# Performance work log

Measured on AMD Instinct MI355X. Metric: run time of the kernel, lower is better.

Reference implementation:

```python
import jax, jax.numpy as jnp
import numpy as np

INPUT_DIM, HIDDEN, LATENT = 17, 512, 256
B, T = 4096, 512


def setup_inputs() -> dict:
    key = jax.random.key(0)
    ks = jax.random.split(key, 16)
    s = 0.02
    inp = {
        "x": jax.random.normal(ks[0], (B, T, INPUT_DIM), dtype=jnp.float32),
        "h0": jnp.zeros((B, HIDDEN), dtype=jnp.float32),
        # encoder: Linear(17->256), ReLU, Linear(256->256), ReLU
        "enc_w1": jax.random.normal(ks[1], (LATENT, INPUT_DIM)) * s,
        "enc_b1": jnp.zeros((LATENT,), jnp.float32),
        "enc_w2": jax.random.normal(ks[2], (LATENT, LATENT)) * s,
        "enc_b2": jnp.zeros((LATENT,), jnp.float32),
        # GRUCell(latent+1 -> hidden): gates ordered [r, z, n] as in torch
        "w_ih": jax.random.normal(ks[3], (3 * HIDDEN, LATENT + 1)) * s,
        "w_hh": jax.random.normal(ks[4], (3 * HIDDEN, HIDDEN)) * s,
        "b_ih": jnp.zeros((3 * HIDDEN,), jnp.float32),
        "b_hh": jnp.zeros((3 * HIDDEN,), jnp.float32),
        "q_w": jax.random.normal(ks[5], (4, HIDDEN)) * s,
        "q_b": jnp.zeros((4,), jnp.float32),
        "v_w": jax.random.normal(ks[6], (3, HIDDEN)) * s,
        "v_b": jnp.zeros((3,), jnp.float32),
        "c_w": jax.random.normal(ks[7], (3, HIDDEN)) * s,
        "c_b": jnp.zeros((3,), jnp.float32),
    }
    return inp


def _quat_to_rotmat(q):
    # q: [B, 4] = [w, x, y, z] -> R: [B, 3, 3]
    w, x, y, z = q[:, 0], q[:, 1], q[:, 2], q[:, 3]
    xx, yy, zz = x * x, y * y, z * z
    xy, xz, yz = x * y, x * z, y * z
    wx, wy, wz = w * x, w * y, w * z
    r0 = jnp.stack([1 - 2 * (yy + zz), 2 * (xy - wz), 2 * (xz + wy)], axis=-1)
    r1 = jnp.stack([2 * (xy + wz), 1 - 2 * (xx + zz), 2 * (yz - wx)], axis=-1)
    r2 = jnp.stack([2 * (xz - wy), 2 * (yz + wx), 1 - 2 * (xx + yy)], axis=-1)
    return jnp.stack([r0, r1, r2], axis=1)


def _gru_cell(xin, h, w_ih, w_hh, b_ih, b_hh):
    gi = xin @ w_ih.T + b_ih  # [B, 3H]
    gh = h @ w_hh.T + b_hh
    i_r, i_z, i_n = jnp.split(gi, 3, axis=-1)
    h_r, h_z, h_n = jnp.split(gh, 3, axis=-1)
    r = jax.nn.sigmoid(i_r + h_r)
    z = jax.nn.sigmoid(i_z + h_z)
    n = jnp.tanh(i_n + r * h_n)
    return (1.0 - z) * n + z * h


def _forward(x, h0, enc_w1, enc_b1, enc_w2, enc_b2, w_ih, w_hh, b_ih, b_hh,
             q_w, q_b, v_w, v_b, c_w, c_b):
    xt = jnp.swapaxes(x, 0, 1)  # [T, B, 17]

    def step(carry, x_t):
        h, dp = carry
        dt = x_t[:, -1:]                      # [B, 1]
        acc = x_t[:, 0:3]                     # [B, 3]
        z1 = jax.nn.relu(x_t @ enc_w1.T + enc_b1)
        lat = jax.nn.relu(z1 @ enc_w2.T + enc_b2)
        gin = jnp.concatenate([lat, dt], axis=-1)
        h = _gru_cell(gin, h, w_ih, w_hh, b_ih, b_hh)
        q_raw = h @ q_w.T + q_b
        # F.normalize(p=2, eps=1e-12)
        q = q_raw / jnp.maximum(jnp.linalg.norm(q_raw, axis=-1, keepdims=True), 1e-12)
        v_world = h @ v_w.T + v_b
        R = _quat_to_rotmat(q)
        acc_world = jnp.einsum('bij,bj->bi', R, acc)
        dp_baseline = v_world * dt + 0.5 * acc_world * dt * dt
        eps = h @ c_w.T + c_b
        dp = dp + dp_baseline + eps
        return (h, dp), None

    total_dp0 = jnp.zeros((x.shape[0], 3), dtype=x.dtype)
    (h_f, total_dp), _ = jax.lax.scan(step, (h0, total_dp0), xt)
    return total_dp


def reference(x, h0, enc_w1, enc_b1, enc_w2, enc_b2, w_ih, w_hh, b_ih, b_hh,
              q_w, q_b, v_w, v_b, c_w, c_b):
    return _forward(x, h0, enc_w1, enc_b1, enc_w2, enc_b2, w_ih, w_hh, b_ih,
                    b_hh, q_w, q_b, v_w, v_b, c_w, c_b)
```

## Files before the change

kernel.cpp:

```cpp
#include <hip/hip_runtime.h>
#include <math.h>

#define T_STEPS 512
#define IN_DIM  17
#define HID     512
#define LAT     256
#define BT      16
#define NTH     512
#define CHUNK   4

typedef __attribute__((ext_vector_type(8))) _Float16 half8;
typedef __attribute__((ext_vector_type(4))) float    f32x4;

#define OFF_HB0   0
#define OFF_HB1   4194304
#define OFF_LAT   8388608
#define OFF_WG    16777216
#define OFF_W2P   19136512
#define OFF_W1P   19267584
#define OFF_HEADP 19283968
#define OFF_W256  19300352
#define OFF_BCOMB 19306496
#define OFF_BHN   19312640
#define OFF_DT    19314688
#define OFF_CTR   19380224

static __device__ inline unsigned short f2h(float f) {
    union { _Float16 h; unsigned short u; } cv;
    cv.h = (_Float16)f;
    return cv.u;
}

__global__ void pack_kernel(const float* __restrict__ enc_w1,
                            const float* __restrict__ enc_w2,
                            const float* __restrict__ w_ih,
                            const float* __restrict__ w_hh,
                            const float* __restrict__ b_ih,
                            const float* __restrict__ b_hh,
                            const float* __restrict__ q_w,
                            const float* __restrict__ v_w,
                            const float* __restrict__ c_w,
                            const float* __restrict__ h0,
                            unsigned char* __restrict__ ws) {
    unsigned short* wgP   = (unsigned short*)(ws + OFF_WG);
    unsigned short* w2P   = (unsigned short*)(ws + OFF_W2P);
    unsigned short* w1P   = (unsigned short*)(ws + OFF_W1P);
    unsigned short* headP = (unsigned short*)(ws + OFF_HEADP);
    unsigned short* hb0   = (unsigned short*)(ws + OFF_HB0);
    float* w256  = (float*)(ws + OFF_W256);
    float* bcomb = (float*)(ws + OFF_BCOMB);
    float* bhn   = (float*)(ws + OFF_BHN);
    unsigned int* ctr = (unsigned int*)(ws + OFF_CTR);

    const int tid = blockIdx.x * blockDim.x + threadIdx.x;
    const int stride = gridDim.x * blockDim.x;

    for (int idx = tid; idx < 32 * 24 * 3 * 64 * 8; idx += stride) {
        int j = idx & 7, l = (idx >> 3) & 63;
        int r = idx >> 9;
        int g = r % 3; r /= 3;
        int kt = r % 24; int s = r / 24;
        int row = g * 512 + s * 16 + (l & 15);
        int kk  = ((l >> 4) & 3) * 8 + j;
        float v;
        if (kt < 8) v = w_ih[(size_t)row * 257 + (kt * 32 + kk)];
        else        v = w_hh[(size_t)row * 512 + ((kt - 8) * 32 + kk)];
        wgP[idx] = f2h(v);
    }
    for (int idx = tid; idx < 16 * 8 * 64 * 8; idx += stride) {
        int j = idx & 7, l = (idx >> 3) & 63, kt = (idx >> 9) & 7, nt = idx >> 12;
        int n = nt * 16 + (l & 15);
        int k = kt * 32 + ((l >> 4) & 3) * 8 + j;
        w2P[idx] = f2h(enc_w2[(size_t)n * 256 + k]);
    }
    for (int idx = tid; idx < 16 * 64 * 8; idx += stride) {
        int j = idx & 7, l = (idx >> 3) & 63, nt = idx >> 9;
        int n = nt * 16 + (l & 15);
        int k = ((l >> 4) & 3) * 8 + j;
        w1P[idx] = (k < IN_DIM) ? f2h(enc_w1[(size_t)n * IN_DIM + k]) : (unsigned short)0;
    }
    for (int idx = tid; idx < 16 * 64 * 8; idx += stride) {
        int j = idx & 7, l = (idx >> 3) & 63, kt = idx >> 9;
        int d = l & 15;
        int k = kt * 32 + ((l >> 4) & 3) * 8 + j;
        float v = 0.f;
        if (d < 4)       v = q_w[(size_t)d * HID + k];
        else if (d < 7)  v = v_w[(size_t)(d - 4) * HID + k];
        else if (d < 10) v = c_w[(size_t)(d - 7) * HID + k];
        headP[idx] = f2h(v);
    }
    for (int idx = tid; idx < 1536; idx += stride) {
        w256[idx]  = w_ih[(size_t)idx * 257 + 256];
        bcomb[idx] = (idx < 1024) ? (b_ih[idx] + b_hh[idx]) : b_ih[idx];
    }
    for (int idx = tid; idx < 512; idx += stride) bhn[idx] = b_hh[1024 + idx];
    for (int idx = tid; idx < 4096 * 512; idx += stride) {
        int c  = idx & 15;
        int r  = (idx >> 4) & 511;
        int sg = idx >> 13;
        int gg = sg >> 5, ss = sg & 31;
        hb0[idx] = f2h(h0[((size_t)(gg * 512 + r)) * 512 + ss * 16 + c]);
    }
    for (int idx = tid; idx < 5128; idx += stride) ctr[idx] = 0;
}

#define MFMA16(a, b, c) __builtin_amdgcn_mfma_f32_16x16x32_f16((a), (b), (c), 0, 0, 0)

static __device__ inline void bar_arrive(unsigned int* slot) {
    __syncthreads();
    if (threadIdx.x == 0)
        __hip_atomic_fetch_add(slot, 1u, __ATOMIC_RELAXED, __HIP_MEMORY_SCOPE_AGENT);
}
static __device__ inline void bar_wait(unsigned int* slot) {
    if (threadIdx.x == 0) {
        unsigned int spins = 0;
        while (__hip_atomic_load(slot, __ATOMIC_RELAXED, __HIP_MEMORY_SCOPE_AGENT) < 32u) {
            __builtin_amdgcn_s_sleep(2);
            if (++spins > 100000000u) break;
        }
    }
    __syncthreads();
    asm volatile("buffer_inv sc0" ::: "memory");
}
static __device__ inline void xcd_barrier(unsigned int* slot) {
    bar_arrive(slot);
    bar_wait(slot);
}

__global__ __launch_bounds__(NTH, 2)
void imu_coop_kernel(const float* __restrict__ x,
                     const float* __restrict__ h0,
                     const float* __restrict__ enc_b1,
                     const float* __restrict__ enc_b2,
                     const float* __restrict__ q_b,
                     const float* __restrict__ v_b,
                     const float* __restrict__ c_b,
                     unsigned char* __restrict__ ws,
                     float* __restrict__ out)
{
    __shared__ __align__(16) unsigned short wgL[24 * 3 * 64 * 8];
    __shared__ __align__(16) unsigned short headL[16 * 64 * 8];
    __shared__ __align__(16) unsigned short xbf64[64][32];
    __shared__ __align__(16) unsigned short z1bf64[64][264];
    __shared__ __align__(16) float          sdotP[8][16][17];
    __shared__ float eb1L[256], eb2L[256];
    __shared__ float dtL[512][4];
    __shared__ float xownL[2][4][16][4];
    __shared__ int   s_slS;

    unsigned short* hb[2] = { (unsigned short*)(ws + OFF_HB0),
                              (unsigned short*)(ws + OFF_HB1) };
    unsigned short*       latbuf = (unsigned short*)(ws + OFF_LAT);
    const unsigned short* wgP    = (const unsigned short*)(ws + OFF_WG);
    const unsigned short* w2P    = (const unsigned short*)(ws + OFF_W2P);
    const unsigned short* w1P    = (const unsigned short*)(ws + OFF_W1P);
    const unsigned short* headP  = (const unsigned short*)(ws + OFF_HEADP);
    const float* w256g = (const float*)(ws + OFF_W256);
    const float* bcmg  = (const float*)(ws + OFF_BCOMB);
    const float* bhng  = (const float*)(ws + OFF_BHN);
    float* dtbuf = (float*)(ws + OFF_DT);

    const int t    = threadIdx.x;
    const int w    = t >> 6;
    const int l    = t & 63;
    const int l15  = l & 15;
    const int lq   = (l >> 4) & 3;
    const int lqh  = lq >> 1;
    const int c8   = (lq & 1) * 8;

    unsigned int xcc;
    asm volatile("s_getreg_b32 %0, hwreg(HW_REG_XCC_ID)" : "=s"(xcc));
    const int g = (int)(xcc & 7u);
    if (t == 0) {
        unsigned int* tk = (unsigned int*)(ws + OFF_CTR) + 5120 + g;
        s_slS = (int)(__hip_atomic_fetch_add(tk, 1u, __ATOMIC_RELAXED,
                                             __HIP_MEMORY_SCOPE_AGENT) & 31u);
    }
    __syncthreads();
    const int s_sl = s_slS;
    const int eb0  = g * 512 + s_sl * 16;

    unsigned int* stepctr  = (unsigned int*)(ws + OFF_CTR) + (size_t)g * 512;
    unsigned int* chunkctr = (unsigned int*)(ws + OFF_CTR + 16384) + (size_t)g * 128;

    const f32x4 fz = {0.f, 0.f, 0.f, 0.f};

    {
        const uint4* src = (const uint4*)(wgP + (size_t)s_sl * (24 * 3 * 64 * 8));
        uint4* dst = (uint4*)wgL;
        for (int i = t; i < 24 * 3 * 64; i += NTH) dst[i] = src[i];
    }
    {
        const uint4* src = (const uint4*)headP;
        uint4* dst = (uint4*)headL;
        for (int i = t; i < 16 * 64; i += NTH) dst[i] = src[i];
    }
    for (int idx = t; idx < 256; idx += NTH) { eb1L[idx] = enc_b1[idx]; eb2L[idx] = enc_b2[idx]; }
    for (int idx = t; idx < 64 * 32; idx += NTH) xbf64[idx >> 5][idx & 31] = 0;

    const float qb0 = q_b[0], qb1 = q_b[1], qb2 = q_b[2], qb3 = q_b[3];
    const float vb0 = v_b[0], vb1 = v_b[1], vb2 = v_b[2];
    const float cb0 = c_b[0], cb1 = c_b[1], cb2 = c_b[2];

    const int jd = s_sl * 16 + l15;
    const float bR  = bcmg[jd],        bZ  = bcmg[512 + jd];
    const float bIN = bcmg[1024 + jd], bHN = bhng[jd];
    const float wr2 = w256g[jd], wz2 = w256g[512 + jd], wn2 = w256g[1024 + jd];

    float ho[4][4];
    #pragma unroll
    for (int mt = 0; mt < 4; ++mt)
        #pragma unroll
        for (int i = 0; i < 4; ++i)
            ho[mt][i] = h0[(size_t)(g * 512 + w * 64 + mt * 16 + lq * 4 + i) * HID + jd];

    float dp0 = 0.f, dp1 = 0.f, dp2 = 0.f;
    __syncthreads();

    const size_t r0 = (size_t)(g * 512 + w * 64) + l15;

#define LDA_L(dst, ktv)                                                         \
            { _Pragma("unroll")                                                 \
              for (int mt = 0; mt < 4; ++mt)                                    \
                  dst[mt] = *(const half8*)(latp + (size_t)mt * (16 * 4 * 256) + (ktv) * 32); }
#define LDA_H(dst, ktv)                                                         \
            { _Pragma("unroll")                                                 \
              for (int mt = 0; mt < 4; ++mt)                                    \
                  dst[mt] = *(const half8*)(hA + (size_t)((ktv) - 8) * 16384 + mt * 256); }
#define LDB(dst, ktv)                                                           \
            { _Pragma("unroll")                                                 \
              for (int gg = 0; gg < 3; ++gg)                                    \
                  dst[gg] = *(const half8*)&wgL[(((ktv) * 3 + gg) * 64 + l) * 8]; }
#define DOMF_L(A, B)                                                            \
            { _Pragma("unroll")                                                 \
              for (int mt = 0; mt < 4; ++mt) {                                  \
                  aR[mt]  = MFMA16(A[mt], B[0], aR[mt]);                        \
                  aZ[mt]  = MFMA16(A[mt], B[1], aZ[mt]);                        \
                  aNi[mt] = MFMA16(A[mt], B[2], aNi[mt]); } }
#define DOMF_H(A, B)                                                            \
            { _Pragma("unroll")                                                 \
              for (int mt = 0; mt < 4; ++mt) {                                  \
                  aR[mt]  = MFMA16(A[mt], B[0], aR[mt]);                        \
                  aZ[mt]  = MFMA16(A[mt], B[1], aZ[mt]);                        \
                  aNh[mt] = MFMA16(A[mt], B[2], aNh[mt]); } }

    for (int s = 0; s < T_STEPS; ++s) {
        const int cs = s & 3;
        const int rp = s & 1, wp = rp ^ 1;
        const unsigned short* hgx = hb[rp] + (size_t)g * 262144;
        unsigned short*       hwx = hb[wp] + (size_t)g * 262144 + (size_t)s_sl * 8192;

        if (cs == 0) {
            if (s > 0) bar_wait(&stepctr[s - 1]);
            const int c = s >> 2;
            for (int idx = t; idx < 17 * 16 * CHUNK; idx += NTH) {
                int k = idx % 17, rem = idx / 17;
                int b = rem & 15, cc = rem >> 4;
                float v = x[((size_t)(eb0 + b) * T_STEPS + (c * 4 + cc)) * IN_DIM + k];
                xbf64[cc * 16 + b][k] = f2h(v);
                if (k < 3) xownL[c & 1][cc][b][k] = v;
                if (k == 16) {
                    dtbuf[(size_t)(eb0 + b) * 4 + cc] = v;
                    xownL[c & 1][cc][b][3] = v;
                }
            }
            __syncthreads();
            {
                const int nt0 = 2 * w, nt1 = 2 * w + 1;
                half8 bv0 = *(const half8*)(w1P + ((size_t)nt0 * 64 + l) * 8);
                half8 bv1 = *(const half8*)(w1P + ((size_t)nt1 * 64 + l) * 8);
                f32x4 e[4][2];
                #pragma unroll
                for (int mt = 0; mt < 4; ++mt) {
                    half8 av = *(const half8*)&xbf64[mt * 16 + l15][lq * 8];
                    e[mt][0] = MFMA16(av, bv0, fz);
                    e[mt][1] = MFMA16(av, bv1, fz);
                }
                __syncthreads();
                #pragma unroll
                for (int mt = 0; mt < 4; ++mt)
                    #pragma unroll
                    for (int i = 0; i < 4; ++i) {
                        int m64 = mt * 16 + lq * 4 + i;
                        int n0 = nt0 * 16 + l15, n1 = nt1 * 16 + l15;
                        z1bf64[m64][n0] = f2h(fmaxf(e[mt][0][i] + eb1L[n0], 0.f));
                        z1bf64[m64][n1] = f2h(fmaxf(e[mt][1][i] + eb1L[n1], 0.f));
                    }
            }
            __syncthreads();
            {
                const int nt0 = 2 * w, nt1 = 2 * w + 1;
                f32x4 e[4][2];
                #pragma unroll
                for (int mt = 0; mt < 4; ++mt) { e[mt][0] = fz; e[mt][1] = fz; }
                #pragma unroll
                for (int kt = 0; kt < 8; ++kt) {
                    half8 bv0 = *(const half8*)(w2P + ((size_t)(nt0 * 8 + kt) * 64 + l) * 8);
                    half8 bv1 = *(const half8*)(w2P + ((size_t)(nt1 * 8 + kt) * 64 + l) * 8);
                    #pragma unroll
                    for (int mt = 0; mt < 4; ++mt) {
                        half8 av = *(const half8*)&z1bf64[mt * 16 + l15][kt * 32 + lq * 8];
                        e[mt][0] = MFMA16(av, bv0, e[mt][0]);
                        e[mt][1] = MFMA16(av, bv1, e[mt][1]);
                    }
                }
                #pragma unroll
                for (int mt = 0; mt < 4; ++mt)
                    #pragma unroll
                    for (int i = 0; i < 4; ++i) {
                        int b = lq * 4 + i;
                        int n0 = nt0 * 16 + l15, n1 = nt1 * 16 + l15;
                        size_t rb = ((size_t)(eb0 + b) * 4 + mt) * 256;
                        latbuf[rb + n0] = f2h(fmaxf(e[mt][0][i] + eb2L[n0], 0.f));
                        latbuf[rb + n1] = f2h(fmaxf(e[mt][1][i] + eb2L[n1], 0.f));
                    }
            }
            xcd_barrier(&chunkctr[c]);
            {
                const float* srcdt = dtbuf + (size_t)g * 2048;
                float* dstdt = &dtL[0][0];
                for (int idx = t; idx < 2048; idx += NTH) dstdt[idx] = srcdt[idx];
            }
            __syncthreads();
        }

        f32x4 aR[4], aZ[4], aNi[4], aNh[4];
        #pragma unroll
        for (int mt = 0; mt < 4; ++mt) { aR[mt] = fz; aZ[mt] = fz; aNi[mt] = fz; aNh[mt] = fz; }

        {
            const unsigned short* latp = latbuf + (r0 * 4 + cs) * 256 + lq * 8;
            half8 aF[3][4], bF[2][3];
            LDA_L(aF[0], 0); LDA_L(aF[1], 1); LDA_L(aF[2], 2);
            LDB(bF[0], 0); LDB(bF[1], 1);
            #pragma unroll
            for (int kt = 0; kt < 8; ++kt) {
                DOMF_L(aF[kt % 3], bF[kt & 1]);
                if (kt < 5) LDA_L(aF[kt % 3], kt + 3);
                if (kt < 6) LDB(bF[kt & 1], kt + 2);
            }
        }

        if (cs != 0 && s > 0) bar_wait(&stepctr[s - 1]);

        const unsigned short* hA = hgx + (size_t)lqh * 8192
                                       + (size_t)(w * 64 + l15) * 16 + c8;
        half8 aF[3][4], bF[2][3];
        LDA_H(aF[0], 8); LDA_H(aF[1], 9); LDA_H(aF[2], 10);
        LDB(bF[0], 8); LDB(bF[1], 9);

        if (s > 0) {
            f32x4 hc = fz;
            const int ka = 2 * w, kb = 2 * w + 1;
            const unsigned short* hH = hgx + (size_t)(s_sl * 16 + l15) * 16 + c8;
            half8 a0 = *(const half8*)(hH + (size_t)(2 * ka + lqh) * 8192);
            half8 b0 = *(const half8*)(headL + ((size_t)ka * 64 + l) * 8);
            half8 a1 = *(const half8*)(hH + (size_t)(2 * kb + lqh) * 8192);
            half8 b1 = *(const half8*)(headL + ((size_t)kb * 64 + l) * 8);
            hc = MFMA16(a0, b0, hc);
            hc = MFMA16(a1, b1, hc);
            #pragma unroll
            for (int i = 0; i < 4; ++i) sdotP[w][lq * 4 + i][l15] = hc[i];
            __syncthreads();
            if (t < BT) {
                const int b = t;
                float sd[10];
                #pragma unroll
                for (int d = 0; d < 10; ++d) {
                    float acc = 0.f;
                    #pragma unroll
                    for (int w8 = 0; w8 < 8; ++w8) acc += sdotP[w8][b][d];
                    sd[d] = acc;
                }
                const int ps = s - 1, pcc = ps & 3, ppar = (ps >> 2) & 1;
                float ax = xownL[ppar][pcc][b][0], ay = xownL[ppar][pcc][b][1];
                float az = xownL[ppar][pcc][b][2], dtv = xownL[ppar][pcc][b][3];
                float q0 = sd[0] + qb0, q1 = sd[1] + qb1;
                float q2 = sd[2] + qb2, q3 = sd[3] + qb3;
                float nrm = fmaxf(sqrtf(q0*q0 + q1*q1 + q2*q2 + q3*q3), 1e-12f);
                float qw = q0/nrm, qx = q1/nrm, qy = q2/nrm, qz = q3/nrm;
                float vx = sd[4] + vb0, vy = sd[5] + vb1, vz = sd[6] + vb2;
                float ex = sd[7] + cb0, ey = sd[8] + cb1, ez = sd[9] + cb2;
                float xx = qx*qx, yy = qy*qy, zz = qz*qz;
                float xy = qx*qy, xz = qx*qz, yz = qy*qz;
                float wxq = qw*qx, wyq = qw*qy, wzq = qw*qz;
                float aw0 = (1.f - 2.f*(yy+zz))*ax + 2.f*(xy-wzq)*ay + 2.f*(xz+wyq)*az;
                float aw1 = 2.f*(xy+wzq)*ax + (1.f - 2.f*(xx+zz))*ay + 2.f*(yz-wxq)*az;
                float aw2 = 2.f*(xz-wyq)*ax + 2.f*(yz+wxq)*ay + (1.f - 2.f*(xx+yy))*az;
                float hdt2 = 0.5f * dtv * dtv;
                dp0 += vx*dtv + aw0*hdt2 + ex;
                dp1 += vy*dtv + aw1*hdt2 + ey;
                dp2 += vz*dtv + aw2*hdt2 + ez;
            }
        }

        #pragma unroll
        for (int k2 = 0; k2 < 16; ++k2) {
            DOMF_H(aF[k2 % 3], bF[k2 & 1]);
            if (k2 < 13) LDA_H(aF[k2 % 3], k2 + 11);
            if (k2 < 14) LDB(bF[k2 & 1], k2 + 10);
        }

        #pragma unroll
        for (int mt = 0; mt < 4; ++mt) {
            #pragma unroll
            for (int i = 0; i < 4; ++i) {
                const int rl = w * 64 + mt * 16 + lq * 4 + i;
                float dtv = dtL[rl][cs];
                float gr = aR[mt][i]  + bR  + dtv * wr2;
                float gz = aZ[mt][i]  + bZ  + dtv * wz2;
                float gi = aNi[mt][i] + bIN + dtv * wn2;
                float gh = aNh[mt][i] + bHN;
                float r  = 1.f / (1.f + __expf(-gr));
                float zg = 1.f / (1.f + __expf(-gz));
                float narg = gi + r * gh;
                float n  = 1.f - 2.f / (__expf(2.f * narg) + 1.f);
                float hn = (1.f - zg) * n + zg * ho[mt][i];
                ho[mt][i] = hn;
                hwx[rl * 16 + l15] = f2h(hn);
            }
        }
        bar_arrive(&stepctr[s]);
    }
#undef LDA_L
#undef LDA_H
#undef LDB
#undef DOMF_L
#undef DOMF_H

    bar_wait(&stepctr[T_STEPS - 1]);
    {
        const unsigned short* hgx = hb[T_STEPS & 1] + (size_t)g * 262144;
        f32x4 hc = fz;
        const int ka = 2 * w, kb = 2 * w + 1;
        const unsigned short* hH = hgx + (size_t)(s_sl * 16 + l15) * 16 + c8;
        half8 a0 = *(const half8*)(hH + (size_t)(2 * ka + lqh) * 8192);
        half8 b0 = *(const half8*)(headL + ((size_t)ka * 64 + l) * 8);
        half8 a1 = *(const half8*)(hH + (size_t)(2 * kb + lqh) * 8192);
        half8 b1 = *(const half8*)(headL + ((size_t)kb * 64 + l) * 8);
        hc = MFMA16(a0, b0, hc);
        hc = MFMA16(a1, b1, hc);
        #pragma unroll
        for (int i = 0; i < 4; ++i) sdotP[w][lq * 4 + i][l15] = hc[i];
    }
    __syncthreads();
    if (t < BT) {
        const int b = t;
        float sd[10];
        #pragma unroll
        for (int d = 0; d < 10; ++d) {
            float acc = 0.f;
            #pragma unroll
            for (int w8 = 0; w8 < 8; ++w8) acc += sdotP[w8][b][d];
            sd[d] = acc;
        }
        const int pcc = (T_STEPS - 1) & 3, ppar = ((T_STEPS - 1) >> 2) & 1;
        float ax = xownL[ppar][pcc][b][0], ay = xownL[ppar][pcc][b][1];
        float az = xownL[ppar][pcc][b][2], dtv = xownL[ppar][pcc][b][3];
        float q0 = sd[0] + qb0, q1 = sd[1] + qb1;
        float q2 = sd[2] + qb2, q3 = sd[3] + qb3;
        float nrm = fmaxf(sqrtf(q0*q0 + q1*q1 + q2*q2 + q3*q3), 1e-12f);
        float qw = q0/nrm, qx = q1/nrm, qy = q2/nrm, qz = q3/nrm;
        float vx = sd[4] + vb0, vy = sd[5] + vb1, vz = sd[6] + vb2;
        float ex = sd[7] + cb0, ey = sd[8] + cb1, ez = sd[9] + cb2;
        float xx = qx*qx, yy = qy*qy, zz = qz*qz;
        float xy = qx*qy, xz = qx*qz, yz = qy*qz;
        float wxq = qw*qx, wyq = qw*qy, wzq = qw*qz;
        float aw0 = (1.f - 2.f*(yy+zz))*ax + 2.f*(xy-wzq)*ay + 2.f*(xz+wyq)*az;
        float aw1 = 2.f*(xy+wzq)*ax + (1.f - 2.f*(xx+zz))*ay + 2.f*(yz-wxq)*az;
        float aw2 = 2.f*(xz-wyq)*ax + 2.f*(yz+wxq)*ay + (1.f - 2.f*(xx+yy))*az;
        float hdt2 = 0.5f * dtv * dtv;
        dp0 += vx*dtv + aw0*hdt2 + ex;
        dp1 += vy*dtv + aw1*hdt2 + ey;
        dp2 += vz*dtv + aw2*hdt2 + ez;
        out[(size_t)(eb0 + b) * 3 + 0] = dp0;
        out[(size_t)(eb0 + b) * 3 + 1] = dp1;
        out[(size_t)(eb0 + b) * 3 + 2] = dp2;
    }
}

extern "C" void kernel_launch(void* const* d_in, const int* in_sizes, int n_in,
                              void* d_out, int out_size, void* d_ws, size_t ws_size,
                              hipStream_t stream) {
    const float* x      = (const float*)d_in[0];
    const float* h0     = (const float*)d_in[1];
    const float* enc_w1 = (const float*)d_in[2];
    const float* enc_b1 = (const float*)d_in[3];
    const float* enc_w2 = (const float*)d_in[4];
    const float* enc_b2 = (const float*)d_in[5];
    const float* w_ih   = (const float*)d_in[6];
    const float* w_hh   = (const float*)d_in[7];
    const float* b_ih   = (const float*)d_in[8];
    const float* b_hh   = (const float*)d_in[9];
    const float* q_w    = (const float*)d_in[10];
    const float* q_b    = (const float*)d_in[11];
    const float* v_w    = (const float*)d_in[12];
    const float* v_b    = (const float*)d_in[13];
    const float* c_w    = (const float*)d_in[14];
    const float* c_b    = (const float*)d_in[15];
    unsigned char* ws = (unsigned char*)d_ws;
    float* out = (float*)d_out;

    hipLaunchKernelGGL(pack_kernel, dim3(2048), dim3(256), 0, stream,
                       enc_w1, enc_w2, w_ih, w_hh, b_ih, b_hh, q_w, v_w, c_w, h0, ws);

    void* args[] = { (void*)&x, (void*)&h0, (void*)&enc_b1, (void*)&enc_b2,
                     (void*)&q_b, (void*)&v_b, (void*)&c_b, (void*)&ws, (void*)&out };
    (void)hipLaunchCooperativeKernel((void*)imu_coop_kernel, dim3(256), dim3(NTH),
                                     args, 0, stream);
}
```

Measured before the change: 12.14 ms.

## Replace counter barriers with per-block tag slots and prefetch encoder chunk

Swaps the atomic-increment step and chunk counters for per-block monotonic tag slots, which 32 lanes poll in parallel, so each barrier costs one plain store instead of a contended atomic add. The encoder MLP for the next chunk now runs right after a step's arrive, overlapping the wait on other blocks, and its results sit in registers until the next chunk's latent write. It also spreads the 10-way head reduction across 160 threads and deepens the h-load prefetch ring from 3 to 4. The cost is more register pressure from the held encoder accumulators and the larger prefetch ring, plus subtle ordering risk around the latent buffer and dt staging.

```diff
diff --git a/kernel.cpp b/kernel.cpp
--- a/kernel.cpp
+++ b/kernel.cpp
@@ -101,30 +101,27 @@
         int gg = sg >> 5, ss = sg & 31;
         hb0[idx] = f2h(h0[((size_t)(gg * 512 + r)) * 512 + ss * 16 + c]);
     }
-    for (int idx = tid; idx < 5128; idx += stride) ctr[idx] = 0;
+    for (int idx = tid; idx < 4096; idx += stride) ctr[idx] = 0;
 }
 
 #define MFMA16(a, b, c) __builtin_amdgcn_mfma_f32_16x16x32_f16((a), (b), (c), 0, 0, 0)
 
-static __device__ inline void bar_arrive(unsigned int* slot) {
+static __device__ inline void tag_arrive(unsigned int* slot, int ss, unsigned int tag) {
     __syncthreads();
     if (threadIdx.x == 0)
-        __hip_atomic_fetch_add(slot, 1u, __ATOMIC_RELAXED, __HIP_MEMORY_SCOPE_AGENT);
+        __hip_atomic_store(slot + ss, tag, __ATOMIC_RELAXED, __HIP_MEMORY_SCOPE_AGENT);
 }
-static __device__ inline void bar_wait(unsigned int* slot) {
-    if (threadIdx.x == 0) {
+static __device__ inline void tag_wait(unsigned int* slot, unsigned int tag) {
+    if (threadIdx.x < 32) {
+        const int lane = (int)threadIdx.x;
         unsigned int spins = 0;
-        while (__hip_atomic_load(slot, __ATOMIC_RELAXED, __HIP_MEMORY_SCOPE_AGENT) < 32u) {
-            __builtin_amdgcn_s_sleep(2);
-            if (++spins > 100000000u) break;
+        while (__hip_atomic_load(slot + lane, __ATOMIC_RELAXED, __HIP_MEMORY_SCOPE_AGENT) < tag) {
+            __builtin_amdgcn_s_sleep(1);
+            if (++spins > 50000000u) break;
         }
     }
     __syncthreads();
     asm volatile("buffer_inv sc0" ::: "memory");
-}
-static __device__ inline void xcd_barrier(unsigned int* slot) {
-    bar_arrive(slot);
-    bar_wait(slot);
 }
 
 __global__ __launch_bounds__(NTH, 2)
@@ -146,6 +143,7 @@
     __shared__ float eb1L[256], eb2L[256];
     __shared__ float dtL[512][4];
     __shared__ float xownL[2][4][16][4];
+    __shared__ float sdS[16][10];
     __shared__ int   s_slS;
 
     unsigned short* hb[2] = { (unsigned short*)(ws + OFF_HB0),
@@ -172,7 +170,7 @@
     asm volatile("s_getreg_b32 %0, hwreg(HW_REG_XCC_ID)" : "=s"(xcc));
     const int g = (int)(xcc & 7u);
     if (t == 0) {
-        unsigned int* tk = (unsigned int*)(ws + OFF_CTR) + 5120 + g;
+        unsigned int* tk = (unsigned int*)(ws + OFF_CTR) + 2048 + g;
         s_slS = (int)(__hip_atomic_fetch_add(tk, 1u, __ATOMIC_RELAXED,
                                              __HIP_MEMORY_SCOPE_AGENT) & 31u);
     }
@@ -180,8 +178,8 @@
     const int s_sl = s_slS;
     const int eb0  = g * 512 + s_sl * 16;
 
-    unsigned int* stepctr  = (unsigned int*)(ws + OFF_CTR) + (size_t)g * 512;
-    unsigned int* chunkctr = (unsigned int*)(ws + OFF_CTR + 16384) + (size_t)g * 128;
+    unsigned int* stepslot  = (unsigned int*)(ws + OFF_CTR) + (size_t)g * 32;
+    unsigned int* chunkslot = (unsigned int*)(ws + OFF_CTR + 4096) + (size_t)g * 32;
 
     const f32x4 fz = {0.f, 0.f, 0.f, 0.f};
 
@@ -215,9 +213,76 @@
             ho[mt][i] = h0[(size_t)(g * 512 + w * 64 + mt * 16 + lq * 4 + i) * HID + jd];
 
     float dp0 = 0.f, dp1 = 0.f, dp2 = 0.f;
+    f32x4 eReg[4][2];
     __syncthreads();
 
     const size_t r0 = (size_t)(g * 512 + w * 64) + l15;
+
+#define STAGE_CHUNK(cchunk)                                                          \
+  { const int c_ = (cchunk);                                                         \
+    for (int idx = t; idx < 17 * 16 * CHUNK; idx += NTH) {                           \
+        int k = idx % 17, rem = idx / 17;                                            \
+        int b = rem & 15, cc = rem >> 4;                                             \
+        float v = x[((size_t)(eb0 + b) * T_STEPS + (c_ * 4 + cc)) * IN_DIM + k];     \
+        xbf64[cc * 16 + b][k] = f2h(v);                                              \
+        if (k < 3) xownL[c_ & 1][cc][b][k] = v;                                      \
+        if (k == 16) {                                                               \
+            dtbuf[(size_t)(eb0 + b) * 4 + cc] = v;                                   \
+            xownL[c_ & 1][cc][b][3] = v;                                             \
+        }                                                                            \
+    }                                                                                \
+    __syncthreads();                                                                 \
+    { const int nt0 = 2 * w, nt1 = 2 * w + 1;                                        \
+      half8 bv0 = *(const half8*)(w1P + ((size_t)nt0 * 64 + l) * 8);                 \
+      half8 bv1 = *(const half8*)(w1P + ((size_t)nt1 * 64 + l) * 8);                 \
+      f32x4 e1[4][2];                                                                \
+      _Pragma("unroll")                                                              \
+      for (int mt = 0; mt < 4; ++mt) {                                               \
+          half8 av = *(const half8*)&xbf64[mt * 16 + l15][lq * 8];                   \
+          e1[mt][0] = MFMA16(av, bv0, fz);                                           \
+          e1[mt][1] = MFMA16(av, bv1, fz);                                           \
+      }                                                                              \
+      __syncthreads();                                                               \
+      _Pragma("unroll")                                                              \
+      for (int mt = 0; mt < 4; ++mt)                                                 \
+          _Pragma("unroll")                                                          \
+          for (int i = 0; i < 4; ++i) {                                              \
+              int m64 = mt * 16 + lq * 4 + i;                                        \
+              int n0 = nt0 * 16 + l15, n1 = nt1 * 16 + l15;                          \
+              z1bf64[m64][n0] = f2h(fmaxf(e1[mt][0][i] + eb1L[n0], 0.f));            \
+              z1bf64[m64][n1] = f2h(fmaxf(e1[mt][1][i] + eb1L[n1], 0.f));            \
+          }                                                                          \
+    }                                                                                \
+    __syncthreads();                                                                 \
+    { const int nt0 = 2 * w, nt1 = 2 * w + 1;                                        \
+      _Pragma("unroll")                                                              \
+      for (int mt = 0; mt < 4; ++mt) { eReg[mt][0] = fz; eReg[mt][1] = fz; }         \
+      _Pragma("unroll")                                                              \
+      for (int kt = 0; kt < 8; ++kt) {                                               \
+          half8 bv0 = *(const half8*)(w2P + ((size_t)(nt0 * 8 + kt) * 64 + l) * 8);  \
+          half8 bv1 = *(const half8*)(w2P + ((size_t)(nt1 * 8 + kt) * 64 + l) * 8);  \
+          _Pragma("unroll")                                                          \
+          for (int mt = 0; mt < 4; ++mt) {                                           \
+              half8 av = *(const half8*)&z1bf64[mt * 16 + l15][kt * 32 + lq * 8];    \
+              eReg[mt][0] = MFMA16(av, bv0, eReg[mt][0]);                            \
+              eReg[mt][1] = MFMA16(av, bv1, eReg[mt][1]);                            \
+          }                                                                          \
+      }                                                                              \
+    }                                                                                \
+  }
+
+#define LATWRITE()                                                                   \
+  { const int nt0 = 2 * w, nt1 = 2 * w + 1;                                          \
+    _Pragma("unroll")                                                                \
+    for (int mt = 0; mt < 4; ++mt)                                                   \
+        _Pragma("unroll")                                                            \
+        for (int i = 0; i < 4; ++i) {                                                \
+            int b = lq * 4 + i;                                                      \
+            int n0 = nt0 * 16 + l15, n1 = nt1 * 16 + l15;                            \
+            size_t rb = ((size_t)(eb0 + b) * 4 + mt) * 256;                          \
+            latbuf[rb + n0] = f2h(fmaxf(eReg[mt][0][i] + eb2L[n0], 0.f));            \
+            latbuf[rb + n1] = f2h(fmaxf(eReg[mt][1][i] + eb2L[n1], 0.f));            \
+        } }
 
 #define LDA_L(dst, ktv)                                                         \
             { _Pragma("unroll")                                                 \
@@ -244,78 +309,29 @@
                   aZ[mt]  = MFMA16(A[mt], B[1], aZ[mt]);                        \
                   aNh[mt] = MFMA16(A[mt], B[2], aNh[mt]); } }
 
+    STAGE_CHUNK(0);
+    LATWRITE();
+    tag_arrive(chunkslot, s_sl, 1u);
+    tag_wait(chunkslot, 1u);
+    {
+        const float* srcdt = dtbuf + (size_t)g * 2048;
+        float* dstdt = &dtL[0][0];
+        for (int idx = t; idx < 2048; idx += NTH) dstdt[idx] = srcdt[idx];
+    }
+    __syncthreads();
+
     for (int s = 0; s < T_STEPS; ++s) {
         const int cs = s & 3;
         const int rp = s & 1, wp = rp ^ 1;
         const unsigned short* hgx = hb[rp] + (size_t)g * 262144;
         unsigned short*       hwx = hb[wp] + (size_t)g * 262144 + (size_t)s_sl * 8192;
 
-        if (cs == 0) {
-            if (s > 0) bar_wait(&stepctr[s - 1]);
+        if (cs == 0 && s > 0) {
             const int c = s >> 2;
-            for (int idx = t; idx < 17 * 16 * CHUNK; idx += NTH) {
-                int k = idx % 17, rem = idx / 17;
-                int b = rem & 15, cc = rem >> 4;
-                float v = x[((size_t)(eb0 + b) * T_STEPS + (c * 4 + cc)) * IN_DIM + k];
-                xbf64[cc * 16 + b][k] = f2h(v);
-                if (k < 3) xownL[c & 1][cc][b][k] = v;
-                if (k == 16) {
-                    dtbuf[(size_t)(eb0 + b) * 4 + cc] = v;
-                    xownL[c & 1][cc][b][3] = v;
-                }
-            }
-            __syncthreads();
-            {
-                const int nt0 = 2 * w, nt1 = 2 * w + 1;
-                half8 bv0 = *(const half8*)(w1P + ((size_t)nt0 * 64 + l) * 8);
-                half8 bv1 = *(const half8*)(w1P + ((size_t)nt1 * 64 + l) * 8);
-                f32x4 e[4][2];
-                #pragma unroll
-                for (int mt = 0; mt < 4; ++mt) {
-                    half8 av = *(const half8*)&xbf64[mt * 16 + l15][lq * 8];
-                    e[mt][0] = MFMA16(av, bv0, fz);
-                    e[mt][1] = MFMA16(av, bv1, fz);
-                }
-                __syncthreads();
-                #pragma unroll
-                for (int mt = 0; mt < 4; ++mt)
-                    #pragma unroll
-                    for (int i = 0; i < 4; ++i) {
-                        int m64 = mt * 16 + lq * 4 + i;
-                        int n0 = nt0 * 16 + l15, n1 = nt1 * 16 + l15;
-                        z1bf64[m64][n0] = f2h(fmaxf(e[mt][0][i] + eb1L[n0], 0.f));
-                        z1bf64[m64][n1] = f2h(fmaxf(e[mt][1][i] + eb1L[n1], 0.f));
-                    }
-            }
-            __syncthreads();
-            {
-                const int nt0 = 2 * w, nt1 = 2 * w + 1;
-                f32x4 e[4][2];
-                #pragma unroll
-                for (int mt = 0; mt < 4; ++mt) { e[mt][0] = fz; e[mt][1] = fz; }
-                #pragma unroll
-                for (int kt = 0; kt < 8; ++kt) {
-                    half8 bv0 = *(const half8*)(w2P + ((size_t)(nt0 * 8 + kt) * 64 + l) * 8);
-                    half8 bv1 = *(const half8*)(w2P + ((size_t)(nt1 * 8 + kt) * 64 + l) * 8);
-                    #pragma unroll
-                    for (int mt = 0; mt < 4; ++mt) {
-                        half8 av = *(const half8*)&z1bf64[mt * 16 + l15][kt * 32 + lq * 8];
-                        e[mt][0] = MFMA16(av, bv0, e[mt][0]);
-                        e[mt][1] = MFMA16(av, bv1, e[mt][1]);
-                    }
-                }
-                #pragma unroll
-                for (int mt = 0; mt < 4; ++mt)
-                    #pragma unroll
-                    for (int i = 0; i < 4; ++i) {
-                        int b = lq * 4 + i;
-                        int n0 = nt0 * 16 + l15, n1 = nt1 * 16 + l15;
-                        size_t rb = ((size_t)(eb0 + b) * 4 + mt) * 256;
-                        latbuf[rb + n0] = f2h(fmaxf(e[mt][0][i] + eb2L[n0], 0.f));
-                        latbuf[rb + n1] = f2h(fmaxf(e[mt][1][i] + eb2L[n1], 0.f));
-                    }
-            }
-            xcd_barrier(&chunkctr[c]);
+            tag_wait(stepslot, (unsigned int)s);
+            LATWRITE();
+            tag_arrive(chunkslot, s_sl, (unsigned int)(c + 1));
+            tag_wait(chunkslot, (unsigned int)(c + 1));
             {
                 const float* srcdt = dtbuf + (size_t)g * 2048;
                 float* dstdt = &dtL[0][0];
@@ -341,13 +357,13 @@
             }
         }
 
-        if (cs != 0 && s > 0) bar_wait(&stepctr[s - 1]);
+        if (cs != 0 && s > 0) tag_wait(stepslot, (unsigned int)s);
 
         const unsigned short* hA = hgx + (size_t)lqh * 8192
                                        + (size_t)(w * 64 + l15) * 16 + c8;
-        half8 aF[3][4], bF[2][3];
-        LDA_H(aF[0], 8); LDA_H(aF[1], 9); LDA_H(aF[2], 10);
-        LDB(bF[0], 8); LDB(bF[1], 9);
+        half8 aH[4][4], bH[2][3];
+        LDA_H(aH[0], 8); LDA_H(aH[1], 9); LDA_H(aH[2], 10); LDA_H(aH[3], 11);
+        LDB(bH[0], 8); LDB(bH[1], 9);
 
         if (s > 0) {
             f32x4 hc = fz;
@@ -362,25 +378,25 @@
             #pragma unroll
             for (int i = 0; i < 4; ++i) sdotP[w][lq * 4 + i][l15] = hc[i];
             __syncthreads();
+            if (t < 160) {
+                const int b = t / 10, d = t % 10;
+                float acc = 0.f;
+                #pragma unroll
+                for (int w8 = 0; w8 < 8; ++w8) acc += sdotP[w8][b][d];
+                sdS[b][d] = acc;
+            }
+            __syncthreads();
             if (t < BT) {
                 const int b = t;
-                float sd[10];
-                #pragma unroll
-                for (int d = 0; d < 10; ++d) {
-                    float acc = 0.f;
-                    #pragma unroll
-                    for (int w8 = 0; w8 < 8; ++w8) acc += sdotP[w8][b][d];
-                    sd[d] = acc;
-                }
                 const int ps = s - 1, pcc = ps & 3, ppar = (ps >> 2) & 1;
                 float ax = xownL[ppar][pcc][b][0], ay = xownL[ppar][pcc][b][1];
                 float az = xownL[ppar][pcc][b][2], dtv = xownL[ppar][pcc][b][3];
-                float q0 = sd[0] + qb0, q1 = sd[1] + qb1;
-                float q2 = sd[2] + qb2, q3 = sd[3] + qb3;
+                float q0 = sdS[b][0] + qb0, q1 = sdS[b][1] + qb1;
+                float q2 = sdS[b][2] + qb2, q3 = sdS[b][3] + qb3;
                 float nrm = fmaxf(sqrtf(q0*q0 + q1*q1 + q2*q2 + q3*q3), 1e-12f);
                 float qw = q0/nrm, qx = q1/nrm, qy = q2/nrm, qz = q3/nrm;
-                float vx = sd[4] + vb0, vy = sd[5] + vb1, vz = sd[6] + vb2;
-                float ex = sd[7] + cb0, ey = sd[8] + cb1, ez = sd[9] + cb2;
+                float vx = sdS[b][4] + vb0, vy = sdS[b][5] + vb1, vz = sdS[b][6] + vb2;
+                float ex = sdS[b][7] + cb0, ey = sdS[b][8] + cb1, ez = sdS[b][9] + cb2;
                 float xx = qx*qx, yy = qy*qy, zz = qz*qz;
                 float xy = qx*qy, xz = qx*qz, yz = qy*qz;
                 float wxq = qw*qx, wyq = qw*qy, wzq = qw*qz;
@@ -396,9 +412,9 @@
 
         #pragma unroll
         for (int k2 = 0; k2 < 16; ++k2) {
-            DOMF_H(aF[k2 % 3], bF[k2 & 1]);
-            if (k2 < 13) LDA_H(aF[k2 % 3], k2 + 11);
-            if (k2 < 14) LDB(bF[k2 & 1], k2 + 10);
+            DOMF_H(aH[k2 & 3], bH[k2 & 1]);
+            if (k2 < 12) LDA_H(aH[k2 & 3], k2 + 12);
+            if (k2 < 14) LDB(bH[k2 & 1], k2 + 10);
         }
 
         #pragma unroll
@@ -420,7 +436,12 @@
                 hwx[rl * 16 + l15] = f2h(hn);
             }
         }
-        bar_arrive(&stepctr[s]);
+        tag_arrive(stepslot, s_sl, (unsigned int)(s + 1));
+
+        if (cs == 3) {
+            const int c = s >> 2;
+            if (c + 1 < T_STEPS / CHUNK) STAGE_CHUNK(c + 1);
+        }
     }
 #undef LDA_L
 #undef LDA_H
@@ -428,7 +449,7 @@
 #undef DOMF_L
 #undef DOMF_H
 
-    bar_wait(&stepctr[T_STEPS - 1]);
+    tag_wait(stepslot, (unsigned int)T_STEPS);
     {
         const unsigned short* hgx = hb[T_STEPS & 1] + (size_t)g * 262144;
         f32x4 hc = fz;
```

Measured after the change: 12.77 ms. +5.2%, slower.
